# Kernel optimization log

Measured on AMD Instinct MI355X. Metric: run time of the kernel, lower is better.

The kernel has to match this reference:

```python
import jax, jax.numpy as jnp
import numpy as np

N, E, F_DIM, H = 50000, 800000, 128, 4


def setup_inputs() -> dict:
    key = jax.random.key(0)
    ks = jax.random.split(key, 12)
    x = jax.random.normal(ks[0], (N, F_DIM), dtype=jnp.float32)
    edge_index = jax.random.randint(ks[1], (2, E), 0, N, dtype=jnp.int64)
    s = 1.0 / np.sqrt(F_DIM)
    return {
        "x": x,
        "edge_index": edge_index,
        "W_gat": jax.random.normal(ks[2], (F_DIM, H * F_DIM), dtype=jnp.float32) * s,
        "att_src": jax.random.normal(ks[3], (H, F_DIM), dtype=jnp.float32) * s,
        "att_dst": jax.random.normal(ks[4], (H, F_DIM), dtype=jnp.float32) * s,
        "bias_gat": jnp.zeros((H * F_DIM,), dtype=jnp.float32),
        "W_mha": jax.random.normal(ks[5], (H * F_DIM, F_DIM), dtype=jnp.float32) * s,
        "b_mha": jnp.zeros((F_DIM,), dtype=jnp.float32),
        "W1": jax.random.normal(ks[6], (F_DIM, F_DIM), dtype=jnp.float32) * s,
        "b1": jnp.zeros((F_DIM,), dtype=jnp.float32),
        "W2": jax.random.normal(ks[7], (F_DIM, F_DIM), dtype=jnp.float32) * s,
        "b2": jnp.zeros((F_DIM,), dtype=jnp.float32),
    }


def gat_conv(x, src, dst, W_gat, att_src, att_dst, bias_gat):
    n = x.shape[0]
    xp = (x @ W_gat).reshape(n, H, F_DIM)            # [N,H,F]
    a_src = jnp.einsum('nhf,hf->nh', xp, att_src)    # [N,H]
    a_dst = jnp.einsum('nhf,hf->nh', xp, att_dst)
    alpha = jax.nn.leaky_relu(a_src[src] + a_dst[dst], 0.2)  # [E,H]
    m = jax.ops.segment_max(alpha, dst, num_segments=n)      # segment softmax over dst
    e = jnp.exp(alpha - m[dst])
    denom = jax.ops.segment_sum(e, dst, num_segments=n)
    att = e / denom[dst]                              # [E,H]
    msg = xp[src] * att[:, :, None]                   # [E,H,F] gather-weight
    out = jax.ops.segment_sum(msg, dst, num_segments=n)  # [N,H,F]
    return out.reshape(n, H * F_DIM) + bias_gat


def reference(x, edge_index, W_gat, att_src, att_dst, bias_gat, W_mha, b_mha, W1, b1, W2, b2):
    n = x.shape[0]
    # PyG GATConv default add_self_loops=True
    ar = jnp.arange(n, dtype=edge_index.dtype)
    src = jnp.concatenate([edge_index[0], ar])
    dst = jnp.concatenate([edge_index[1], ar])
    residual = x
    h = jax.nn.leaky_relu(gat_conv(x, src, dst, W_gat, att_src, att_dst, bias_gat), 0.01)
    h = h @ W_mha + b_mha + residual
    # Ffn
    res2 = h
    h = jax.nn.leaky_relu(h @ W1 + b1, 0.01)
    h = h @ W2 + b2 + res2
    return h
```

## Files before the change

### kernel.cpp

```cpp
#include <hip/hip_runtime.h>

#define FD 128
#define NH 4
#define HF 512
#define CAP 24

typedef __attribute__((ext_vector_type(8))) short short8;
typedef __attribute__((ext_vector_type(4))) float v4f;

__device__ __forceinline__ float lrelu(float x, float s) { return x > 0.f ? x : s * x; }

__device__ __forceinline__ unsigned short f2bf(float f) {
    unsigned int u = __float_as_uint(f);
    u += 0x7FFFu + ((u >> 16) & 1u);
    return (unsigned short)(u >> 16);
}
__device__ __forceinline__ unsigned int pack2(float a, float b) {
    return (unsigned)f2bf(a) | ((unsigned)f2bf(b) << 16);
}

__global__ __launch_bounds__(256) void k_prep(const float* __restrict__ x,
                                              unsigned short* __restrict__ xb,
                                              const float* __restrict__ Wg, unsigned short* __restrict__ WgT,
                                              const float* __restrict__ Wm, unsigned short* __restrict__ WmT,
                                              const float* __restrict__ W1, unsigned short* __restrict__ W1T,
                                              const float* __restrict__ W2, unsigned short* __restrict__ W2T,
                                              const float* __restrict__ att_s,
                                              const float* __restrict__ att_d,
                                              float* __restrict__ U, int n) {
    const int t = threadIdx.x;
    int b = blockIdx.x;
    const int nCast = (n * FD / 8 + 255) / 256;
    const int nT1 = (FD * HF / 4 + 255) / 256;
    const int nT3 = (FD * FD / 4 + 255) / 256;
    if (b < nCast) {
        int i = b * 256 + t;
        if (i < n * FD / 8) {
            const float4* x4 = reinterpret_cast<const float4*>(x);
            float4 v0 = x4[i * 2], v1 = x4[i * 2 + 1];
            uint4 o;
            o.x = pack2(v0.x, v0.y); o.y = pack2(v0.z, v0.w);
            o.z = pack2(v1.x, v1.y); o.w = pack2(v1.z, v1.w);
            reinterpret_cast<uint4*>(xb)[i] = o;
        }
        return;
    }
    b -= nCast;
    if (b < nT1) {
        int i4 = (b * 256 + t) * 4;
        if (i4 < FD * HF) {
            int nn = i4 >> 7, k = i4 & 127;
            uint2 o;
            o.x = pack2(Wg[(size_t)k * HF + nn], Wg[(size_t)(k + 1) * HF + nn]);
            o.y = pack2(Wg[(size_t)(k + 2) * HF + nn], Wg[(size_t)(k + 3) * HF + nn]);
            *reinterpret_cast<uint2*>(&WgT[i4]) = o;
        }
        return;
    }
    b -= nT1;
    if (b < nT1) {
        int i4 = (b * 256 + t) * 4;
        if (i4 < HF * FD) {
            int nn = i4 >> 9, k = i4 & 511;
            uint2 o;
            o.x = pack2(Wm[(size_t)k * FD + nn], Wm[(size_t)(k + 1) * FD + nn]);
            o.y = pack2(Wm[(size_t)(k + 2) * FD + nn], Wm[(size_t)(k + 3) * FD + nn]);
            *reinterpret_cast<uint2*>(&WmT[i4]) = o;
        }
        return;
    }
    b -= nT1;
    if (b < nT3) {
        int i4 = (b * 256 + t) * 4;
        if (i4 < FD * FD) {
            int nn = i4 >> 7, k = i4 & 127;
            uint2 o;
            o.x = pack2(W1[(size_t)k * FD + nn], W1[(size_t)(k + 1) * FD + nn]);
            o.y = pack2(W1[(size_t)(k + 2) * FD + nn], W1[(size_t)(k + 3) * FD + nn]);
            *reinterpret_cast<uint2*>(&W1T[i4]) = o;
        }
        return;
    }
    b -= nT3;
    if (b < nT3) {
        int i4 = (b * 256 + t) * 4;
        if (i4 < FD * FD) {
            int nn = i4 >> 7, k = i4 & 127;
            uint2 o;
            o.x = pack2(W2[(size_t)k * FD + nn], W2[(size_t)(k + 1) * FD + nn]);
            o.y = pack2(W2[(size_t)(k + 2) * FD + nn], W2[(size_t)(k + 3) * FD + nn]);
            *reinterpret_cast<uint2*>(&W2T[i4]) = o;
        }
        return;
    }
    b -= nT3;
    {
        int idx = b * 256 + t;
        if (idx < 1024) {
            int type = idx >> 9, h = (idx >> 7) & 3, k = idx & 127;
            const float* att = type ? att_d : att_s;
            const float* wrow = &Wg[(size_t)k * HF + h * FD];
            const float* arow = &att[h * FD];
            float s = 0.f;
#pragma unroll 4
            for (int j = 0; j < FD; ++j) s += wrow[j] * arow[j];
            U[idx] = s;
        }
    }
}

__global__ __launch_bounds__(256) void k_alog(const unsigned short* __restrict__ xb,
                                              const float* __restrict__ U,
                                              float* __restrict__ a_s,
                                              float* __restrict__ a_d, int n) {
    int idx = blockIdx.x * 256 + threadIdx.x;
    int node = idx >> 2, h = idx & 3;
    if (node >= n) return;
    const uint4* xr = reinterpret_cast<const uint4*>(&xb[(size_t)node * FD]);
    const float* us = &U[h * FD];
    const float* ud = &U[512 + h * FD];
    float ps = 0.f, pd = 0.f;
#pragma unroll 4
    for (int j = 0; j < 16; ++j) {
        uint4 u = xr[j];
        const unsigned w[4] = {u.x, u.y, u.z, u.w};
#pragma unroll
        for (int q = 0; q < 4; ++q) {
            float f0 = __uint_as_float(w[q] << 16);
            float f1 = __uint_as_float(w[q] & 0xffff0000u);
            int c = j * 8 + q * 2;
            ps += f0 * us[c] + f1 * us[c + 1];
            pd += f0 * ud[c] + f1 * ud[c + 1];
        }
    }
    a_s[node * NH + h] = ps;
    a_d[node * NH + h] = pd;
}

__global__ __launch_bounds__(256) void k_scatter(const int* __restrict__ es,
                                                 const int* __restrict__ ed,
                                                 const float* __restrict__ a_s,
                                                 const float* __restrict__ a_d,
                                                 int* __restrict__ cur,
                                                 uint4* __restrict__ edata, int E, int n) {
    int i = blockIdx.x * 256 + threadIdx.x;
    if (i >= E) return;
    int s = es[i], d = ed[i];
    const float4 as = *reinterpret_cast<const float4*>(&a_s[(size_t)s * NH]);
    const float4 ad = *reinterpret_cast<const float4*>(&a_d[(size_t)d * NH]);
    float w0 = __expf(lrelu(as.x + ad.x, 0.2f));
    float w1 = __expf(lrelu(as.y + ad.y, 0.2f));
    float w2 = __expf(lrelu(as.z + ad.z, 0.2f));
    float w3 = __expf(lrelu(as.w + ad.w, 0.2f));
    int sub = i & 3;
    int pos = atomicAdd(&cur[sub * n + d], 1);
    if (pos < CAP) {
        uint4 r;
        r.x = (unsigned)s;
        r.y = pack2(w0, w1);
        r.z = pack2(w2, w3);
        r.w = 0u;
        edata[(size_t)d * (4 * CAP) + sub * CAP + pos] = r;
    }
}

#define EDGE_BODY(REC) do {                                                    \
    int s_ = (int)(REC).x;                                                     \
    float w0_ = __uint_as_float((REC).y << 16);                                \
    float w1_ = __uint_as_float((REC).y & 0xffff0000u);                        \
    float w2_ = __uint_as_float((REC).z << 16);                                \
    float w3_ = __uint_as_float((REC).z & 0xffff0000u);                        \
    unsigned u_ = *reinterpret_cast<const unsigned*>(&xb[(size_t)s_ * FD + 2 * l]); \
    float g0_ = __uint_as_float(u_ << 16);                                     \
    float g1_ = __uint_as_float(u_ & 0xffff0000u);                             \
    ax0 += g0_ * w0_; ay0 += g1_ * w0_; den0 += w0_;                           \
    ax1 += g0_ * w1_; ay1 += g1_ * w1_; den1 += w1_;                           \
    ax2 += g0_ * w2_; ay2 += g1_ * w2_; den2 += w2_;                           \
    ax3 += g0_ * w3_; ay3 += g1_ * w3_; den3 += w3_;                           \
} while (0)

__global__ __launch_bounds__(256, 8) void k_aggr2(const unsigned short* __restrict__ xb,
                                                  const float* __restrict__ a_s,
                                                  const float* __restrict__ a_d,
                                                  const int* __restrict__ cur,
                                                  const uint4* __restrict__ edata,
                                                  unsigned short* __restrict__ agg, int n) {
    const int wv = threadIdx.x >> 6, l = threadIdx.x & 63;
    const int node = blockIdx.x * 4 + wv;
    if (node >= n) return;

    const float4 as4 = *reinterpret_cast<const float4*>(&a_s[(size_t)node * NH]);
    const float4 ad4 = *reinterpret_cast<const float4*>(&a_d[(size_t)node * NH]);
    const float wS0 = __expf(lrelu(as4.x + ad4.x, 0.2f));
    const float wS1 = __expf(lrelu(as4.y + ad4.y, 0.2f));
    const float wS2 = __expf(lrelu(as4.z + ad4.z, 0.2f));
    const float wS3 = __expf(lrelu(as4.w + ad4.w, 0.2f));

    float ax0, ay0, ax1, ay1, ax2, ay2, ax3, ay3;
    float den0 = wS0, den1 = wS1, den2 = wS2, den3 = wS3;
    {
        unsigned ux = *reinterpret_cast<const unsigned*>(&xb[(size_t)node * FD + 2 * l]);
        float f0 = __uint_as_float(ux << 16);
        float f1 = __uint_as_float(ux & 0xffff0000u);
        ax0 = f0 * wS0; ay0 = f1 * wS0;
        ax1 = f0 * wS1; ay1 = f1 * wS1;
        ax2 = f0 * wS2; ay2 = f1 * wS2;
        ax3 = f0 * wS3; ay3 = f1 * wS3;
    }

    const uint4* edp = edata + (size_t)node * (4 * CAP);
#pragma unroll
    for (int sub = 0; sub < 4; ++sub) {
        int deg = __builtin_amdgcn_readfirstlane(cur[sub * n + node]);
        deg = min(deg, CAP);
        const uint4* p = edp + sub * CAP;
        int e = 0;
        for (; e + 4 <= deg; e += 4) {
            uint4 r0 = p[e], r1 = p[e + 1], r2 = p[e + 2], r3 = p[e + 3];
            EDGE_BODY(r0); EDGE_BODY(r1); EDGE_BODY(r2); EDGE_BODY(r3);
        }
        for (; e < deg; ++e) {
            uint4 r0 = p[e];
            EDGE_BODY(r0);
        }
    }

    const float i0 = 1.f / den0, i1 = 1.f / den1, i2 = 1.f / den2, i3 = 1.f / den3;
    unsigned* ag = reinterpret_cast<unsigned*>(&agg[(size_t)node * HF + 2 * l]);
    ag[0]      = pack2(ax0 * i0, ay0 * i0);
    ag[64]     = pack2(ax1 * i1, ay1 * i1);
    ag[128]    = pack2(ax2 * i2, ay2 * i2);
    ag[192]    = pack2(ax3 * i3, ay3 * i3);
}

#define PREFETCH8(BP, STRIDE) do {                                             \
    _Pragma("unroll")                                                          \
    for (int rnd = 0; rnd < 8; ++rnd) {                                        \
        int r_ = rnd * 16 + sr;                                                \
        R[rnd] = *reinterpret_cast<const short8*>(&(BP)[(size_t)r_ * (STRIDE) + sc]); \
    } } while (0)

#define COMMIT8() do {                                                         \
    __syncthreads();                                                           \
    _Pragma("unroll")                                                          \
    for (int rnd = 0; rnd < 8; ++rnd) {                                        \
        int r_ = rnd * 16 + sr;                                                \
        *reinterpret_cast<short8*>(&WL[r_][sc]) = R[rnd];                      \
    }                                                                          \
    __syncthreads(); } while (0)

#define LOAD_A(HH) do {                                                        \
    _Pragma("unroll")                                                          \
    for (int kk = 0; kk < 4; ++kk) {                                           \
        RA0[kk] = *reinterpret_cast<const short8*>(                            \
            &agg[(size_t)amr0 * HF + (HH) * FD + kk * 32 + kg]);               \
        RA1[kk] = *reinterpret_cast<const short8*>(                            \
            &agg[(size_t)amr1 * HF + (HH) * FD + kk * 32 + kg]);               \
    } } while (0)

__global__ __launch_bounds__(256, 2) void k_tail(const unsigned short* __restrict__ agg,
                                                 const unsigned short* __restrict__ WgT,
                                                 const float* __restrict__ biasg,
                                                 const unsigned short* __restrict__ WmT,
                                                 const float* __restrict__ bm,
                                                 const float* __restrict__ x,
                                                 const unsigned short* __restrict__ W1T,
                                                 const float* __restrict__ b1,
                                                 const unsigned short* __restrict__ W2T,
                                                 const float* __restrict__ b2,
                                                 float* __restrict__ out, int n) {
    __shared__ unsigned short WL[128][132];
    __shared__ unsigned short tS[128][132];
    const int tid = threadIdx.x;
    const int m0 = blockIdx.x * 128;
    const int wv = tid >> 6, l = tid & 63;
    const int rA = l & 15;
    const int kg = (l >> 4) * 8;
    const int mw = m0 + wv * 32;
    const int amr0 = min(mw + rA, n - 1);
    const int amr1 = min(mw + 16 + rA, n - 1);
    const int sr = tid >> 4, sc = (tid & 15) * 8;

    short8 R[8];
    short8 RA0[4], RA1[4];
    v4f hma[2][8];
#pragma unroll
    for (int g = 0; g < 2; ++g)
#pragma unroll
        for (int t = 0; t < 8; ++t) hma[g][t] = (v4f){0.f, 0.f, 0.f, 0.f};

    LOAD_A(0);
    PREFETCH8(WgT, FD);

#pragma unroll
    for (int h = 0; h < 4; ++h) {
        COMMIT8();
        PREFETCH8(WmT + h * FD, HF);
        v4f acc[2][8];
#pragma unroll
        for (int g = 0; g < 2; ++g)
#pragma unroll
            for (int t = 0; t < 8; ++t) acc[g][t] = (v4f){0.f, 0.f, 0.f, 0.f};
        __builtin_amdgcn_s_setprio(1);
#pragma unroll
        for (int kk = 0; kk < 4; ++kk) {
#pragma unroll
            for (int nt = 0; nt < 8; ++nt) {
                short8 b = *reinterpret_cast<const short8*>(&WL[nt * 16 + rA][kk * 32 + kg]);
                acc[0][nt] = __builtin_amdgcn_mfma_f32_16x16x32_bf16(RA0[kk], b, acc[0][nt], 0, 0, 0);
                acc[1][nt] = __builtin_amdgcn_mfma_f32_16x16x32_bf16(RA1[kk], b, acc[1][nt], 0, 0, 0);
            }
        }
        __builtin_amdgcn_s_setprio(0);
#pragma unroll
        for (int g = 0; g < 2; ++g)
#pragma unroll
            for (int nt = 0; nt < 8; ++nt) {
                const int col = nt * 16 + rA;
                const float bv = biasg[h * FD + col];
#pragma unroll
                for (int i = 0; i < 4; ++i)
                    tS[wv * 32 + g * 16 + (l >> 4) * 4 + i][col] =
                        f2bf(lrelu(acc[g][nt][i] + bv, 0.01f));
            }
        COMMIT8();
        PREFETCH8((h < 3 ? WgT + (h + 1) * FD * FD : W1T), FD);
        if (h < 3) LOAD_A(h + 1);
        __builtin_amdgcn_s_setprio(1);
#pragma unroll
        for (int kk = 0; kk < 4; ++kk) {
            short8 a0 = *reinterpret_cast<const short8*>(&tS[wv * 32 + rA][kk * 32 + kg]);
            short8 a1 = *reinterpret_cast<const short8*>(&tS[wv * 32 + 16 + rA][kk * 32 + kg]);
#pragma unroll
            for (int nt = 0; nt < 8; ++nt) {
                short8 b = *reinterpret_cast<const short8*>(&WL[nt * 16 + rA][kk * 32 + kg]);
                hma[0][nt] = __builtin_amdgcn_mfma_f32_16x16x32_bf16(a0, b, hma[0][nt], 0, 0, 0);
                hma[1][nt] = __builtin_amdgcn_mfma_f32_16x16x32_bf16(a1, b, hma[1][nt], 0, 0, 0);
            }
        }
        __builtin_amdgcn_s_setprio(0);
    }

#pragma unroll
    for (int g = 0; g < 2; ++g)
#pragma unroll
        for (int nt = 0; nt < 8; ++nt) {
            const int col = nt * 16 + rA;
            const float bv = bm[col];
#pragma unroll
            for (int i = 0; i < 4; ++i) {
                const int r = min(mw + g * 16 + (l >> 4) * 4 + i, n - 1);
                float v = hma[g][nt][i] + bv + x[(size_t)r * FD + col];
                hma[g][nt][i] = v;
                tS[wv * 32 + g * 16 + (l >> 4) * 4 + i][col] = f2bf(v);
            }
        }
    COMMIT8();
    PREFETCH8(W2T, FD);
    v4f acc[2][8];
#pragma unroll
    for (int g = 0; g < 2; ++g)
#pragma unroll
        for (int t = 0; t < 8; ++t) acc[g][t] = (v4f){0.f, 0.f, 0.f, 0.f};
    __builtin_amdgcn_s_setprio(1);
#pragma unroll
    for (int kk = 0; kk < 4; ++kk) {
        short8 a0 = *reinterpret_cast<const short8*>(&tS[wv * 32 + rA][kk * 32 + kg]);
        short8 a1 = *reinterpret_cast<const short8*>(&tS[wv * 32 + 16 + rA][kk * 32 + kg]);
#pragma unroll
        for (int nt = 0; nt < 8; ++nt) {
            short8 b = *reinterpret_cast<const short8*>(&WL[nt * 16 + rA][kk * 32 + kg]);
            acc[0][nt] = __builtin_amdgcn_mfma_f32_16x16x32_bf16(a0, b, acc[0][nt], 0, 0, 0);
            acc[1][nt] = __builtin_amdgcn_mfma_f32_16x16x32_bf16(a1, b, acc[1][nt], 0, 0, 0);
        }
    }
    __builtin_amdgcn_s_setprio(0);
#pragma unroll
    for (int g = 0; g < 2; ++g)
#pragma unroll
        for (int nt = 0; nt < 8; ++nt) {
            const int col = nt * 16 + rA;
            const float bv = b1[col];
#pragma unroll
            for (int i = 0; i < 4; ++i)
                tS[wv * 32 + g * 16 + (l >> 4) * 4 + i][col] =
                    f2bf(lrelu(acc[g][nt][i] + bv, 0.01f));
        }
    COMMIT8();
#pragma unroll
    for (int g = 0; g < 2; ++g)
#pragma unroll
        for (int t = 0; t < 8; ++t) acc[g][t] = (v4f){0.f, 0.f, 0.f, 0.f};
    __builtin_amdgcn_s_setprio(1);
#pragma unroll
    for (int kk = 0; kk < 4; ++kk) {
        short8 a0 = *reinterpret_cast<const short8*>(&tS[wv * 32 + rA][kk * 32 + kg]);
        short8 a1 = *reinterpret_cast<const short8*>(&tS[wv * 32 + 16 + rA][kk * 32 + kg]);
#pragma unroll
        for (int nt = 0; nt < 8; ++nt) {
            short8 b = *reinterpret_cast<const short8*>(&WL[nt * 16 + rA][kk * 32 + kg]);
            acc[0][nt] = __builtin_amdgcn_mfma_f32_16x16x32_bf16(a0, b, acc[0][nt], 0, 0, 0);
            acc[1][nt] = __builtin_amdgcn_mfma_f32_16x16x32_bf16(a1, b, acc[1][nt], 0, 0, 0);
        }
    }
    __builtin_amdgcn_s_setprio(0);
#pragma unroll
    for (int g = 0; g < 2; ++g)
#pragma unroll
        for (int nt = 0; nt < 8; ++nt) {
            const int col = nt * 16 + rA;
            const float bv = b2[col];
#pragma unroll
            for (int i = 0; i < 4; ++i) {
                const int r = mw + g * 16 + (l >> 4) * 4 + i;
                if (r < n)
                    out[(size_t)r * FD + col] = acc[g][nt][i] + bv + hma[g][nt][i];
            }
        }
}

extern "C" void kernel_launch(void* const* d_in, const int* in_sizes, int n_in,
                              void* d_out, int out_size, void* d_ws, size_t ws_size,
                              hipStream_t stream) {
    const float* x     = (const float*)d_in[0];
    const int*   ei    = (const int*)d_in[1];
    const float* Wg    = (const float*)d_in[2];
    const float* att_s = (const float*)d_in[3];
    const float* att_d = (const float*)d_in[4];
    const float* biasg = (const float*)d_in[5];
    const float* Wm    = (const float*)d_in[6];
    const float* bm    = (const float*)d_in[7];
    const float* W1    = (const float*)d_in[8];
    const float* b1    = (const float*)d_in[9];
    const float* W2    = (const float*)d_in[10];
    const float* b2    = (const float*)d_in[11];
    float* out = (float*)d_out;

    const int n = in_sizes[0] / FD;
    const int E = in_sizes[1] / 2;
    const int* esrc = ei;
    const int* edst = ei + E;

    char* w = (char*)d_ws;
    size_t o = 0;
    auto alloc = [&](size_t b) { void* p = w + o; o = (o + b + 255) & ~(size_t)255; return p; };
    unsigned short* x_b  = (unsigned short*)alloc((size_t)n * FD * 2);
    unsigned short* WgT  = (unsigned short*)alloc((size_t)FD * HF * 2);
    unsigned short* WmT  = (unsigned short*)alloc((size_t)HF * FD * 2);
    unsigned short* W1T  = (unsigned short*)alloc((size_t)FD * FD * 2);
    unsigned short* W2T  = (unsigned short*)alloc((size_t)FD * FD * 2);
    float*          U    = (float*)alloc(1024 * 4);
    unsigned short* aggb = (unsigned short*)alloc((size_t)n * HF * 2);
    float* a_s   = (float*)alloc((size_t)n * NH * 4);
    float* a_d   = (float*)alloc((size_t)n * NH * 4);
    int*   cur   = (int*)alloc((size_t)n * 4 * 4);
    uint4* edata = (uint4*)alloc((size_t)n * (4 * CAP) * 16);

    hipMemsetAsync(cur, 0, (size_t)n * 4 * 4, stream);

    const int nCast = (n * FD / 8 + 255) / 256;
    const int nT1 = (FD * HF / 4 + 255) / 256;
    const int nT3 = (FD * FD / 4 + 255) / 256;
    k_prep<<<nCast + 2 * nT1 + 2 * nT3 + 4, 256, 0, stream>>>(
        x, x_b, Wg, WgT, Wm, WmT, W1, W1T, W2, W2T, att_s, att_d, U, n);

    k_alog<<<(n * 4 + 255) / 256, 256, 0, stream>>>(x_b, U, a_s, a_d, n);

    k_scatter<<<(E + 255) / 256, 256, 0, stream>>>(esrc, edst, a_s, a_d, cur, edata, E, n);
    k_aggr2<<<(n + 3) / 4, 256, 0, stream>>>(x_b, a_s, a_d, cur, edata, aggb, n);

    const int mb2 = (n + 127) / 128;
    k_tail<<<mb2, 256, 0, stream>>>(aggb, WgT, biasg, WmT, bm, x, W1T, b1, W2T, b2, out, n);
}
```

Measured before the change: 203.3 us.

## Use 8 per-block edge buckets and stage edge records in LDS before aggregation

The scatter kernel now picks the bucket from the block index across 8 sub-buckets of capacity 16, and the counters are interleaved per node, so the 8 counters of one node sit together in memory. In the aggregation kernel each wave first loads all bucket records in parallel into a shared-memory slab, compacting them, then loops over the compacted list using packed float2 accumulators. This aims to cut the serialized dependent global loads per bucket and improve counter locality. In exchange the edata buffer and memset grow, LDS use per block rises, and occupancy may drop.

```diff
diff --git a/kernel.cpp b/kernel.cpp
--- a/kernel.cpp
+++ b/kernel.cpp
@@ -3,10 +3,12 @@
 #define FD 128
 #define NH 4
 #define HF 512
-#define CAP 24
+#define SUBS 8
+#define CAP 16
 
 typedef __attribute__((ext_vector_type(8))) short short8;
 typedef __attribute__((ext_vector_type(4))) float v4f;
+typedef __attribute__((ext_vector_type(2))) float v2f;
 
 __device__ __forceinline__ float lrelu(float x, float s) { return x > 0.f ? x : s * x; }
 
@@ -145,6 +147,7 @@
                                                  uint4* __restrict__ edata, int E, int n) {
     int i = blockIdx.x * 256 + threadIdx.x;
     if (i >= E) return;
+    const int sub = blockIdx.x & (SUBS - 1);
     int s = es[i], d = ed[i];
     const float4 as = *reinterpret_cast<const float4*>(&a_s[(size_t)s * NH]);
     const float4 ad = *reinterpret_cast<const float4*>(&a_d[(size_t)d * NH]);
@@ -152,31 +155,27 @@
     float w1 = __expf(lrelu(as.y + ad.y, 0.2f));
     float w2 = __expf(lrelu(as.z + ad.z, 0.2f));
     float w3 = __expf(lrelu(as.w + ad.w, 0.2f));
-    int sub = i & 3;
-    int pos = atomicAdd(&cur[sub * n + d], 1);
+    int pos = atomicAdd(&cur[d * SUBS + sub], 1);
     if (pos < CAP) {
         uint4 r;
         r.x = (unsigned)s;
         r.y = pack2(w0, w1);
         r.z = pack2(w2, w3);
         r.w = 0u;
-        edata[(size_t)d * (4 * CAP) + sub * CAP + pos] = r;
-    }
-}
-
-#define EDGE_BODY(REC) do {                                                    \
+        edata[(size_t)d * (SUBS * CAP) + sub * CAP + pos] = r;
+    }
+}
+
+#define EB(REC) do {                                                           \
     int s_ = (int)(REC).x;                                                     \
     float w0_ = __uint_as_float((REC).y << 16);                                \
     float w1_ = __uint_as_float((REC).y & 0xffff0000u);                        \
     float w2_ = __uint_as_float((REC).z << 16);                                \
     float w3_ = __uint_as_float((REC).z & 0xffff0000u);                        \
     unsigned u_ = *reinterpret_cast<const unsigned*>(&xb[(size_t)s_ * FD + 2 * l]); \
-    float g0_ = __uint_as_float(u_ << 16);                                     \
-    float g1_ = __uint_as_float(u_ & 0xffff0000u);                             \
-    ax0 += g0_ * w0_; ay0 += g1_ * w0_; den0 += w0_;                           \
-    ax1 += g0_ * w1_; ay1 += g1_ * w1_; den1 += w1_;                           \
-    ax2 += g0_ * w2_; ay2 += g1_ * w2_; den2 += w2_;                           \
-    ax3 += g0_ * w3_; ay3 += g1_ * w3_; den3 += w3_;                           \
+    v2f g_; g_.x = __uint_as_float(u_ << 16); g_.y = __uint_as_float(u_ & 0xffff0000u); \
+    acc0 += g_ * w0_; acc1 += g_ * w1_; acc2 += g_ * w2_; acc3 += g_ * w3_;    \
+    d01 += (v2f){w0_, w1_}; d23 += (v2f){w2_, w3_};                            \
 } while (0)
 
 __global__ __launch_bounds__(256, 8) void k_aggr2(const unsigned short* __restrict__ xb,
@@ -185,6 +184,7 @@
                                                   const int* __restrict__ cur,
                                                   const uint4* __restrict__ edata,
                                                   unsigned short* __restrict__ agg, int n) {
+    __shared__ uint4 slab[4][SUBS * CAP];
     const int wv = threadIdx.x >> 6, l = threadIdx.x & 63;
     const int node = blockIdx.x * 4 + wv;
     if (node >= n) return;
@@ -196,41 +196,42 @@
     const float wS2 = __expf(lrelu(as4.z + ad4.z, 0.2f));
     const float wS3 = __expf(lrelu(as4.w + ad4.w, 0.2f));
 
-    float ax0, ay0, ax1, ay1, ax2, ay2, ax3, ay3;
-    float den0 = wS0, den1 = wS1, den2 = wS2, den3 = wS3;
+    const uint4* edp = edata + (size_t)node * (SUBS * CAP);
+    int base = 0;
+#pragma unroll
+    for (int sub = 0; sub < SUBS; ++sub) {
+        int dg = __builtin_amdgcn_readfirstlane(cur[node * SUBS + sub]);
+        dg = min(dg, CAP);
+        if (l < dg) slab[wv][base + l] = edp[sub * CAP + l];
+        base += dg;
+    }
+    const int deg = base;
+
+    v2f acc0, acc1, acc2, acc3, d01, d23;
     {
         unsigned ux = *reinterpret_cast<const unsigned*>(&xb[(size_t)node * FD + 2 * l]);
-        float f0 = __uint_as_float(ux << 16);
-        float f1 = __uint_as_float(ux & 0xffff0000u);
-        ax0 = f0 * wS0; ay0 = f1 * wS0;
-        ax1 = f0 * wS1; ay1 = f1 * wS1;
-        ax2 = f0 * wS2; ay2 = f1 * wS2;
-        ax3 = f0 * wS3; ay3 = f1 * wS3;
-    }
-
-    const uint4* edp = edata + (size_t)node * (4 * CAP);
-#pragma unroll
-    for (int sub = 0; sub < 4; ++sub) {
-        int deg = __builtin_amdgcn_readfirstlane(cur[sub * n + node]);
-        deg = min(deg, CAP);
-        const uint4* p = edp + sub * CAP;
-        int e = 0;
-        for (; e + 4 <= deg; e += 4) {
-            uint4 r0 = p[e], r1 = p[e + 1], r2 = p[e + 2], r3 = p[e + 3];
-            EDGE_BODY(r0); EDGE_BODY(r1); EDGE_BODY(r2); EDGE_BODY(r3);
-        }
-        for (; e < deg; ++e) {
-            uint4 r0 = p[e];
-            EDGE_BODY(r0);
-        }
-    }
-
-    const float i0 = 1.f / den0, i1 = 1.f / den1, i2 = 1.f / den2, i3 = 1.f / den3;
+        v2f g; g.x = __uint_as_float(ux << 16); g.y = __uint_as_float(ux & 0xffff0000u);
+        acc0 = g * wS0; acc1 = g * wS1; acc2 = g * wS2; acc3 = g * wS3;
+        d01 = (v2f){wS0, wS1}; d23 = (v2f){wS2, wS3};
+    }
+
+    const uint4* sl = slab[wv];
+    int e = 0;
+    for (; e + 4 <= deg; e += 4) {
+        uint4 r0 = sl[e], r1 = sl[e + 1], r2 = sl[e + 2], r3 = sl[e + 3];
+        EB(r0); EB(r1); EB(r2); EB(r3);
+    }
+    for (; e < deg; ++e) {
+        uint4 r0 = sl[e];
+        EB(r0);
+    }
+
+    const float i0 = 1.f / d01.x, i1 = 1.f / d01.y, i2 = 1.f / d23.x, i3 = 1.f / d23.y;
     unsigned* ag = reinterpret_cast<unsigned*>(&agg[(size_t)node * HF + 2 * l]);
-    ag[0]      = pack2(ax0 * i0, ay0 * i0);
-    ag[64]     = pack2(ax1 * i1, ay1 * i1);
-    ag[128]    = pack2(ax2 * i2, ay2 * i2);
-    ag[192]    = pack2(ax3 * i3, ay3 * i3);
+    ag[0]   = pack2(acc0.x * i0, acc0.y * i0);
+    ag[64]  = pack2(acc1.x * i1, acc1.y * i1);
+    ag[128] = pack2(acc2.x * i2, acc2.y * i2);
+    ag[192] = pack2(acc3.x * i3, acc3.y * i3);
 }
 
 #define PREFETCH8(BP, STRIDE) do {                                             \
@@ -453,10 +454,10 @@
     unsigned short* aggb = (unsigned short*)alloc((size_t)n * HF * 2);
     float* a_s   = (float*)alloc((size_t)n * NH * 4);
     float* a_d   = (float*)alloc((size_t)n * NH * 4);
-    int*   cur   = (int*)alloc((size_t)n * 4 * 4);
-    uint4* edata = (uint4*)alloc((size_t)n * (4 * CAP) * 16);
-
-    hipMemsetAsync(cur, 0, (size_t)n * 4 * 4, stream);
+    int*   cur   = (int*)alloc((size_t)n * SUBS * 4);
+    uint4* edata = (uint4*)alloc((size_t)n * (SUBS * CAP) * 16);
+
+    hipMemsetAsync(cur, 0, (size_t)n * SUBS * 4, stream);
 
     const int nCast = (n * FD / 8 + 255) / 256;
     const int nT1 = (FD * HF / 4 + 255) / 256;
```

New measurement: 198.7 us. 1.02x faster.
